# Kernel optimization log

Measured on AMD Instinct MI355X. Metric: run time of the kernel, lower is better.

Reference implementation:

```python
import jax, jax.numpy as jnp
import numpy as np

N_NODES = 20000
N_EDGES = 320000
N_GRAPHS = 512
IN_FEATS = 128
HID = 256
RDKIT_IN = 2048
RDK_H1, RDK_H2 = 1024, 512
COMB_H1, COMB_H2 = 1024, 512
N_TASKS = 1
EPS = 1e-5


def _lin(k, fan_in, fan_out):
    return jax.random.normal(k, (fan_in, fan_out), jnp.float32) / np.float32(np.sqrt(fan_in))


def setup_inputs() -> dict:
    key = jax.random.key(0)
    ks = jax.random.split(key, 24)
    inp = {}
    inp["node_feats"] = jax.random.normal(ks[0], (N_NODES, IN_FEATS), jnp.float32)
    inp["rdkit_feats"] = jax.random.normal(ks[1], (N_GRAPHS, RDKIT_IN), jnp.float32)
    inp["src"] = jax.random.randint(ks[2], (N_EDGES,), 0, N_NODES, dtype=jnp.int32)
    inp["dst"] = jax.random.randint(ks[3], (N_EDGES,), 0, N_NODES, dtype=jnp.int32)
    # sorted graph ids; first N_GRAPHS entries guarantee every graph has >=1 node
    gid = jnp.concatenate([jnp.arange(N_GRAPHS, dtype=jnp.int32),
                           jax.random.randint(ks[4], (N_NODES - N_GRAPHS,), 0, N_GRAPHS, dtype=jnp.int32)])
    inp["node_gid"] = jnp.sort(gid)
    # GCN layer params (GraphConv W,b + residual Linear + BatchNorm gamma/beta)
    dims = [(IN_FEATS, HID), (HID, HID)]
    for i, (fi, fo) in enumerate(dims, start=1):
        inp[f"W{i}"] = _lin(ks[4 + 4 * i], fi, fo)
        inp[f"b{i}"] = jnp.zeros((fo,), jnp.float32)
        inp[f"rW{i}"] = _lin(ks[5 + 4 * i], fi, fo)
        inp[f"rb{i}"] = jnp.zeros((fo,), jnp.float32)
        inp[f"g{i}"] = jnp.ones((fo,), jnp.float32)
        inp[f"be{i}"] = jnp.zeros((fo,), jnp.float32)
    inp["aw_W"] = _lin(ks[16], HID, 1)
    inp["aw_b"] = jnp.zeros((1,), jnp.float32)
    inp["rk_W1"] = _lin(ks[17], RDKIT_IN, RDK_H1)
    inp["rk_b1"] = jnp.zeros((RDK_H1,), jnp.float32)
    inp["rk_W2"] = _lin(ks[18], RDK_H1, RDK_H2)
    inp["rk_b2"] = jnp.zeros((RDK_H2,), jnp.float32)
    comb_in = RDK_H2 + 2 * HID
    inp["c_W1"] = _lin(ks[19], comb_in, COMB_H1)
    inp["c_b1"] = jnp.zeros((COMB_H1,), jnp.float32)
    inp["c_W2"] = _lin(ks[20], COMB_H1, COMB_H2)
    inp["c_b2"] = jnp.zeros((COMB_H2,), jnp.float32)
    inp["c_W3"] = _lin(ks[21], COMB_H2, N_TASKS)
    inp["c_b3"] = jnp.zeros((N_TASKS,), jnp.float32)
    return inp


def _gcn_layer(h, src, dst, W, b, rW, rb, g, be):
    # GraphConv, norm='none': sum incoming messages of (X W), then bias + relu
    m = h @ W                                                    # [N, out]
    agg = jax.ops.segment_sum(m[src], dst, num_segments=h.shape[0])
    new = jax.nn.relu(agg + b)
    # residual Linear with activation (dgllife GCNLayer)
    new = new + jax.nn.relu(h @ rW + rb)
    # BatchNorm1d over nodes (training-mode batch stats; dropout in eval = identity)
    mu = new.mean(axis=0)
    var = new.var(axis=0)
    return g * (new - mu) * jax.lax.rsqrt(var + EPS) + be


def reference(node_feats, rdkit_feats, src, dst, node_gid,
              W1, b1, rW1, rb1, g1, be1,
              W2, b2, rW2, rb2, g2, be2,
              aw_W, aw_b, rk_W1, rk_b1, rk_W2, rk_b2,
              c_W1, c_b1, c_W2, c_b2, c_W3, c_b3):
    h = _gcn_layer(node_feats, src, dst, W1, b1, rW1, rb1, g1, be1)
    h = _gcn_layer(h, src, dst, W2, b2, rW2, rb2, g2, be2)
    # WeightedSumAndMax readout
    w = jax.nn.sigmoid(h @ aw_W + aw_b)                          # [N, 1]
    hg_sum = jax.ops.segment_sum(h * w, node_gid, num_segments=N_GRAPHS)
    hg_max = jax.ops.segment_max(h, node_gid, num_segments=N_GRAPHS)
    graph_feats = jnp.concatenate([hg_sum, hg_max], axis=1)       # [B, 2*HID]
    # RDKit encoder MLP
    r = jax.nn.relu(rdkit_feats @ rk_W1 + rk_b1)
    r = jax.nn.relu(r @ rk_W2 + rk_b2)
    z = jnp.concatenate([graph_feats, r], axis=1)
    z = jax.nn.relu(z @ c_W1 + c_b1)
    z = jax.nn.relu(z @ c_W2 + c_b2)
    return z @ c_W3 + c_b3                                       # [B, n_tasks]
```

## Files before the change

kernel.cpp:

```cpp
#include <hip/hip_runtime.h>
#include <hip/hip_bf16.h>
#include <cstdint>
#include <cstddef>

#define N_NODES 20000
#define N_EDGES 320000
#define N_GRAPHS 512
#define IN_FEATS 128
#define HID 256

typedef __bf16 bhalf;
typedef __bf16 bhalf8 __attribute__((ext_vector_type(8)));
typedef __bf16 bhalf4 __attribute__((ext_vector_type(4)));
typedef __bf16 bhalf2 __attribute__((ext_vector_type(2)));
typedef float f32x4 __attribute__((ext_vector_type(4)));

template<int RELU, int OUTBF16>
__global__ __launch_bounds__(256) void gemm_mfma(const bhalf* __restrict__ A,
                                                 const bhalf* __restrict__ Bt,
                                                 void* __restrict__ Cv,
                                                 const float* __restrict__ bias,
                                                 int M, int K, int ldc)
{
    __shared__ bhalf As[64 * 64];
    __shared__ bhalf Bs[64 * 64];

    const int t = threadIdx.x;
    const int lane = t & 63, wid = t >> 6;
    const int wm0 = (wid >> 1) * 32, wn0 = (wid & 1) * 32;
    const int m0 = blockIdx.y * 64, n0 = blockIdx.x * 64;
    const int S = gridDim.z, kz = blockIdx.z;
    const int Ks = K / S;

    const int srow = t >> 2;
    const int sc0 = (t & 3) << 3;

    f32x4 acc[2][2] = {};
    uint4 ra0, ra1, rb0, rb1;

    const bool mok = (m0 + srow) < M;
    const bhalf* Abase = A + (size_t)(m0 + srow) * K + (size_t)kz * Ks;
    const bhalf* Bbase = Bt + (size_t)(n0 + srow) * K + (size_t)kz * Ks;

    ra0 = mok ? *(const uint4*)(Abase + sc0)      : make_uint4(0u,0u,0u,0u);
    ra1 = mok ? *(const uint4*)(Abase + sc0 + 32) : make_uint4(0u,0u,0u,0u);
    rb0 = *(const uint4*)(Bbase + sc0);
    rb1 = *(const uint4*)(Bbase + sc0 + 32);

    const int swz = (srow & 7) << 3;
    for (int k0 = 0; k0 < Ks; k0 += 64) {
        __syncthreads();
        *(uint4*)&As[srow * 64 + (sc0 ^ swz)]        = ra0;
        *(uint4*)&As[srow * 64 + ((sc0 + 32) ^ swz)] = ra1;
        *(uint4*)&Bs[srow * 64 + (sc0 ^ swz)]        = rb0;
        *(uint4*)&Bs[srow * 64 + ((sc0 + 32) ^ swz)] = rb1;
        __syncthreads();
        if (k0 + 64 < Ks) {
            const bhalf* An = Abase + k0 + 64;
            const bhalf* Bn = Bbase + k0 + 64;
            ra0 = mok ? *(const uint4*)(An + sc0)      : make_uint4(0u,0u,0u,0u);
            ra1 = mok ? *(const uint4*)(An + sc0 + 32) : make_uint4(0u,0u,0u,0u);
            rb0 = *(const uint4*)(Bn + sc0);
            rb1 = *(const uint4*)(Bn + sc0 + 32);
        }
#pragma unroll
        for (int kb = 0; kb < 2; ++kb) {
            const int kc = kb * 32 + (lane >> 4) * 8;
            bhalf8 af[2], bfr[2];
#pragma unroll
            for (int i = 0; i < 2; ++i) {
                int rA = wm0 + i * 16 + (lane & 15);
                af[i] = *(const bhalf8*)&As[rA * 64 + (kc ^ ((rA & 7) << 3))];
                int rB = wn0 + i * 16 + (lane & 15);
                bfr[i] = *(const bhalf8*)&Bs[rB * 64 + (kc ^ ((rB & 7) << 3))];
            }
#pragma unroll
            for (int mi = 0; mi < 2; ++mi)
#pragma unroll
                for (int ni = 0; ni < 2; ++ni)
                    acc[mi][ni] = __builtin_amdgcn_mfma_f32_16x16x32_bf16(
                        af[mi], bfr[ni], acc[mi][ni], 0, 0, 0);
        }
    }

#pragma unroll
    for (int mi = 0; mi < 2; ++mi)
#pragma unroll
        for (int ni = 0; ni < 2; ++ni) {
            int col = n0 + wn0 + ni * 16 + (lane & 15);
            f32x4 v = acc[mi][ni];
            if (S > 1) {
#pragma unroll
                for (int r = 0; r < 4; ++r) {
                    int row = m0 + wm0 + mi * 16 + (lane >> 4) * 4 + r;
                    if (row < M)
                        ((float*)Cv)[((size_t)kz * M + row) * ldc + col] = v[r];
                }
            } else {
                float bb = bias ? bias[col] : 0.f;
#pragma unroll
                for (int r = 0; r < 4; ++r) {
                    int row = m0 + wm0 + mi * 16 + (lane >> 4) * 4 + r;
                    if (row < M) {
                        float x = v[r] + bb;
                        if (RELU) x = fmaxf(x, 0.f);
                        if (OUTBF16) ((bhalf*)Cv)[(size_t)row * ldc + col] = (bhalf)x;
                        else         ((float*)Cv)[(size_t)row * ldc + col] = x;
                    }
                }
            }
        }
}

__global__ __launch_bounds__(256) void gcn_gemm_fused(const bhalf* __restrict__ Aagg,
                                                      const bhalf* __restrict__ Ax,
                                                      const bhalf* __restrict__ BW,
                                                      const bhalf* __restrict__ BrW,
                                                      const float* __restrict__ b,
                                                      const float* __restrict__ rb,
                                                      bhalf* __restrict__ vout,
                                                      float* __restrict__ stats,
                                                      int M, int K)
{
    __shared__ bhalf As[64 * 64];
    __shared__ bhalf Bs[64 * 64];
    __shared__ float ssum[64], ssq[64];

    const int t = threadIdx.x;
    const int lane = t & 63, wid = t >> 6;
    const int wm0 = (wid >> 1) * 32, wn0 = (wid & 1) * 32;
    const int m0 = blockIdx.y * 64, n0 = blockIdx.x * 64;

    const int srow = t >> 2;
    const int sc0 = (t & 3) << 3;
    const int nk = K >> 6;

    f32x4 accM[2][2] = {};
    f32x4 accR[2][2] = {};
    uint4 ra0, ra1, rb0, rb1;

    const bool mok = (m0 + srow) < M;
    const bhalf* A0r = Aagg + (size_t)(m0 + srow) * K;
    const bhalf* A1r = Ax + (size_t)(m0 + srow) * K;
    const bhalf* B0r = BW + (size_t)(n0 + srow) * K;
    const bhalf* B1r = BrW + (size_t)(n0 + srow) * K;

    ra0 = mok ? *(const uint4*)(A0r + sc0)      : make_uint4(0u,0u,0u,0u);
    ra1 = mok ? *(const uint4*)(A0r + sc0 + 32) : make_uint4(0u,0u,0u,0u);
    rb0 = *(const uint4*)(B0r + sc0);
    rb1 = *(const uint4*)(B0r + sc0 + 32);

    const int swz = (srow & 7) << 3;
    const int total = 2 * nk;
    for (int ii = 0; ii < total; ++ii) {
        __syncthreads();
        *(uint4*)&As[srow * 64 + (sc0 ^ swz)]        = ra0;
        *(uint4*)&As[srow * 64 + ((sc0 + 32) ^ swz)] = ra1;
        *(uint4*)&Bs[srow * 64 + (sc0 ^ swz)]        = rb0;
        *(uint4*)&Bs[srow * 64 + ((sc0 + 32) ^ swz)] = rb1;
        __syncthreads();
        int jj = ii + 1;
        if (jj < total) {
            bool seln = jj >= nk;
            int kk = (seln ? jj - nk : jj) << 6;
            const bhalf* Ab = (seln ? A1r : A0r) + kk;
            const bhalf* Bb = (seln ? B1r : B0r) + kk;
            ra0 = mok ? *(const uint4*)(Ab + sc0)      : make_uint4(0u,0u,0u,0u);
            ra1 = mok ? *(const uint4*)(Ab + sc0 + 32) : make_uint4(0u,0u,0u,0u);
            rb0 = *(const uint4*)(Bb + sc0);
            rb1 = *(const uint4*)(Bb + sc0 + 32);
        }
        const bool selc = ii >= nk;
#pragma unroll
        for (int kb = 0; kb < 2; ++kb) {
            const int kc = kb * 32 + (lane >> 4) * 8;
            bhalf8 af[2], bfr[2];
#pragma unroll
            for (int i = 0; i < 2; ++i) {
                int rA = wm0 + i * 16 + (lane & 15);
                af[i] = *(const bhalf8*)&As[rA * 64 + (kc ^ ((rA & 7) << 3))];
                int rB = wn0 + i * 16 + (lane & 15);
                bfr[i] = *(const bhalf8*)&Bs[rB * 64 + (kc ^ ((rB & 7) << 3))];
            }
            if (!selc) {
#pragma unroll
                for (int mi = 0; mi < 2; ++mi)
#pragma unroll
                    for (int ni = 0; ni < 2; ++ni)
                        accM[mi][ni] = __builtin_amdgcn_mfma_f32_16x16x32_bf16(
                            af[mi], bfr[ni], accM[mi][ni], 0, 0, 0);
            } else {
#pragma unroll
                for (int mi = 0; mi < 2; ++mi)
#pragma unroll
                    for (int ni = 0; ni < 2; ++ni)
                        accR[mi][ni] = __builtin_amdgcn_mfma_f32_16x16x32_bf16(
                            af[mi], bfr[ni], accR[mi][ni], 0, 0, 0);
            }
        }
    }

    if (t < 64) { ssum[t] = 0.f; ssq[t] = 0.f; }
    __syncthreads();
    float sloc[2] = {0.f, 0.f}, s2loc[2] = {0.f, 0.f};
#pragma unroll
    for (int ni = 0; ni < 2; ++ni) {
        int cl = wn0 + ni * 16 + (lane & 15);
        int c = n0 + cl;
        float bb = b[c], rbb = rb[c];
#pragma unroll
        for (int mi = 0; mi < 2; ++mi) {
            f32x4 a0v = accM[mi][ni], a1v = accR[mi][ni];
#pragma unroll
            for (int r = 0; r < 4; ++r) {
                int row = m0 + wm0 + mi * 16 + (lane >> 4) * 4 + r;
                if (row < M) {
                    float x = fmaxf(a0v[r] + bb, 0.f) + fmaxf(a1v[r] + rbb, 0.f);
                    vout[(size_t)row * HID + c] = (bhalf)x;
                    sloc[ni] += x;
                    s2loc[ni] += x * x;
                }
            }
        }
        atomicAdd(&ssum[cl], sloc[ni]);
        atomicAdd(&ssq[cl], s2loc[ni]);
    }
    __syncthreads();
    if (t < 64) {
        atomicAdd(&stats[n0 + t], ssum[t]);
        atomicAdd(&stats[HID + n0 + t], ssq[t]);
    }
}

template<int RELU, int OUTBF16>
__global__ __launch_bounds__(256) void splitk_combine(const float* __restrict__ part,
                                                      int S, int M, int N, int ldo,
                                                      const float* __restrict__ bias,
                                                      void* __restrict__ outv)
{
    int i = blockIdx.x * blockDim.x + threadIdx.x;
    int n4 = N >> 2;
    if (i >= M * n4) return;
    int row = i / n4, c4 = (i - row * n4) << 2;
    float4 s = make_float4(0.f, 0.f, 0.f, 0.f);
    for (int z = 0; z < S; ++z) {
        float4 p = *(const float4*)(part + ((size_t)z * M + row) * N + c4);
        s.x += p.x; s.y += p.y; s.z += p.z; s.w += p.w;
    }
    float4 bb = *(const float4*)(bias + c4);
    s.x += bb.x; s.y += bb.y; s.z += bb.z; s.w += bb.w;
    if (RELU) {
        s.x = fmaxf(s.x, 0.f); s.y = fmaxf(s.y, 0.f);
        s.z = fmaxf(s.z, 0.f); s.w = fmaxf(s.w, 0.f);
    }
    if (OUTBF16) {
        bhalf4 o = {(bhalf)s.x, (bhalf)s.y, (bhalf)s.z, (bhalf)s.w};
        *(bhalf4*)((bhalf*)outv + (size_t)row * ldo + c4) = o;
    } else {
        *(float4*)((float*)outv + (size_t)row * ldo + c4) = s;
    }
}

__global__ __launch_bounds__(128) void splitk_combine_dot(const float* __restrict__ part,
                                                          int S, int M, int N,
                                                          const float* __restrict__ bias,
                                                          const float* __restrict__ W3,
                                                          const float* __restrict__ b3,
                                                          float* __restrict__ out)
{
    int row = blockIdx.x, t = threadIdx.x;
    int c4 = t << 2;
    float4 s = make_float4(0.f, 0.f, 0.f, 0.f);
    for (int z = 0; z < S; ++z) {
        float4 p = *(const float4*)(part + ((size_t)z * M + row) * N + c4);
        s.x += p.x; s.y += p.y; s.z += p.z; s.w += p.w;
    }
    float4 bb = *(const float4*)(bias + c4);
    float4 w = *(const float4*)(W3 + c4);
    float d = fmaxf(s.x + bb.x, 0.f) * w.x + fmaxf(s.y + bb.y, 0.f) * w.y
            + fmaxf(s.z + bb.z, 0.f) * w.z + fmaxf(s.w + bb.w, 0.f) * w.w;
#pragma unroll
    for (int off = 32; off > 0; off >>= 1) d += __shfl_xor(d, off);
    __shared__ float ws2[2];
    if ((t & 63) == 0) ws2[t >> 6] = d;
    __syncthreads();
    if (t == 0) out[row] = ws2[0] + ws2[1] + b3[0];
}

struct WEnt { const float* src; bhalf* dst; int K; int N; int tiles_end; };
struct WTab { WEnt e[8]; };

__global__ __launch_bounds__(256) void wconv_batch(WTab tab)
{
    __shared__ float tile[32][33];
    int tb = blockIdx.x;
    int idx = 0;
#pragma unroll
    for (int i = 0; i < 8; ++i)
        if (tb >= tab.e[i].tiles_end) idx = i + 1;
    const WEnt& E = tab.e[idx];
    int t0 = idx ? tab.e[idx - 1].tiles_end : 0;
    int lt = tb - t0;
    int tX = E.N >> 5;
    int bx = (lt % tX) << 5;
    int by = (lt / tX) << 5;
    int tx = threadIdx.x & 31, ty = threadIdx.x >> 5;
#pragma unroll
    for (int i = 0; i < 32; i += 8)
        tile[ty + i][tx] = E.src[(size_t)(by + ty + i) * E.N + bx + tx];
    __syncthreads();
#pragma unroll
    for (int i = 0; i < 32; i += 8)
        E.dst[(size_t)(bx + ty + i) * E.K + by + tx] = (bhalf)tile[tx][ty + i];
}

__global__ void conv_batch(const float* __restrict__ a, bhalf* __restrict__ oa, int n4a,
                           const float* __restrict__ b, bhalf* __restrict__ ob, int n4b)
{
    int i = blockIdx.x * blockDim.x + threadIdx.x;
    const float* s; bhalf* d; int j;
    if (i < n4a) { s = a; d = oa; j = i; }
    else { j = i - n4a; if (j >= n4b) return; s = b; d = ob; }
    float4 v = ((const float4*)s)[j];
    bhalf4 o = {(bhalf)v.x, (bhalf)v.y, (bhalf)v.z, (bhalf)v.w};
    ((bhalf4*)d)[j] = o;
}

__global__ void csr_count(const int* __restrict__ dst, int* __restrict__ counts)
{
    int e = blockIdx.x * blockDim.x + threadIdx.x;
    if (e >= N_EDGES) return;
    atomicAdd(&counts[dst[e]], 1);
}

__global__ __launch_bounds__(256) void csr_scan_a(const int* __restrict__ counts,
                                                  int* __restrict__ bsum)
{
    int i = blockIdx.x * 256 + threadIdx.x;
    int v = (i < N_NODES) ? counts[i] : 0;
#pragma unroll
    for (int off = 32; off > 0; off >>= 1) v += __shfl_down(v, off);
    __shared__ int ws[4];
    if ((threadIdx.x & 63) == 0) ws[threadIdx.x >> 6] = v;
    __syncthreads();
    if (threadIdx.x == 0) bsum[blockIdx.x] = ws[0] + ws[1] + ws[2] + ws[3];
}

__global__ __launch_bounds__(128) void csr_scan_b(int* __restrict__ bsum, int nb)
{
    __shared__ int tmp[128];
    int t = threadIdx.x;
    tmp[t] = (t < nb) ? bsum[t] : 0;
    __syncthreads();
    if (t == 0) {
        int run = 0;
        for (int i = 0; i < nb; ++i) { int c = tmp[i]; tmp[i] = run; run += c; }
    }
    __syncthreads();
    if (t < nb) bsum[t] = tmp[t];
}

__global__ __launch_bounds__(256) void csr_scan_c(const int* __restrict__ counts,
                                                  const int* __restrict__ bsum,
                                                  int* __restrict__ offsets)
{
    int t = threadIdx.x, b = blockIdx.x;
    int i = b * 256 + t;
    int v = (i < N_NODES) ? counts[i] : 0;
    int x = v;
#pragma unroll
    for (int off = 1; off < 64; off <<= 1) {
        int y = __shfl_up(x, off);
        if ((t & 63) >= off) x += y;
    }
    __shared__ int wsum[4];
    if ((t & 63) == 63) wsum[t >> 6] = x;
    __syncthreads();
    int add = bsum[b];
    for (int w = 0; w < (t >> 6); ++w) add += wsum[w];
    int excl = x - v + add;
    if (i < N_NODES) offsets[i] = excl;
    if (i == N_NODES - 1) offsets[N_NODES] = excl + v;
}

__global__ void csr_fill(const int* __restrict__ src, const int* __restrict__ dst,
                         const int* __restrict__ offsets, int* __restrict__ cursor,
                         int* __restrict__ eidx)
{
    int e = blockIdx.x * blockDim.x + threadIdx.x;
    if (e >= N_EDGES) return;
    int d = dst[e];
    int slot = offsets[d] + atomicAdd(&cursor[d], 1);
    eidx[slot] = src[e];
}

__global__ void csr_sort_wave(const int* __restrict__ offsets, int* __restrict__ eidx)
{
    int gidx = blockIdx.x * blockDim.x + threadIdx.x;
    int n = gidx >> 6, lane = gidx & 63;
    if (n >= N_NODES) return;
    int lo = offsets[n], hi = offsets[n + 1];
    int cnt = hi - lo;
    if (cnt <= 1) return;
    if (cnt <= 64) {
        int v = (lane < cnt) ? eidx[lo + lane] : 0x7fffffff;
        int rank = 0;
        for (int j = 0; j < cnt; ++j) {
            int vj = __shfl(v, j);
            if (vj < v || (vj == v && j < lane)) ++rank;
        }
        if (lane < cnt) eidx[lo + rank] = v;
    } else if (lane == 0) {
        for (int i = lo + 1; i < hi; ++i) {
            int v = eidx[i]; int j = i - 1;
            while (j >= lo && eidx[j] > v) { eidx[j + 1] = eidx[j]; --j; }
            eidx[j + 1] = v;
        }
    }
}

template<int COLS>
__global__ __launch_bounds__(256) void edge_gather_b(const bhalf* __restrict__ m,
                                                     const int* __restrict__ offsets,
                                                     const int* __restrict__ eidx,
                                                     bhalf* __restrict__ agg)
{
    int gidx = blockIdx.x * blockDim.x + threadIdx.x;
    int n = gidx >> 6, lane = gidx & 63;
    if (n >= N_NODES) return;
    int lo = offsets[n], hi = offsets[n + 1];
    if (COLS == 256) {
        const bhalf* base = m + lane * 4;
        float4 acc = make_float4(0.f, 0.f, 0.f, 0.f);
        int i = lo;
        for (; i + 2 <= hi; i += 2) {
            bhalf4 v0 = *(const bhalf4*)(base + (size_t)eidx[i] * COLS);
            bhalf4 v1 = *(const bhalf4*)(base + (size_t)eidx[i + 1] * COLS);
            acc.x += (float)v0.x + (float)v1.x;
            acc.y += (float)v0.y + (float)v1.y;
            acc.z += (float)v0.z + (float)v1.z;
            acc.w += (float)v0.w + (float)v1.w;
        }
        if (i < hi) {
            bhalf4 v0 = *(const bhalf4*)(base + (size_t)eidx[i] * COLS);
            acc.x += (float)v0.x; acc.y += (float)v0.y;
            acc.z += (float)v0.z; acc.w += (float)v0.w;
        }
        bhalf4 o = {(bhalf)acc.x, (bhalf)acc.y, (bhalf)acc.z, (bhalf)acc.w};
        *(bhalf4*)(agg + (size_t)n * COLS + lane * 4) = o;
    } else {
        const bhalf* base = m + lane * 2;
        float ax = 0.f, ay = 0.f;
        int i = lo;
        for (; i + 2 <= hi; i += 2) {
            bhalf2 v0 = *(const bhalf2*)(base + (size_t)eidx[i] * COLS);
            bhalf2 v1 = *(const bhalf2*)(base + (size_t)eidx[i + 1] * COLS);
            ax += (float)v0.x + (float)v1.x;
            ay += (float)v0.y + (float)v1.y;
        }
        if (i < hi) {
            bhalf2 v0 = *(const bhalf2*)(base + (size_t)eidx[i] * COLS);
            ax += (float)v0.x; ay += (float)v0.y;
        }
        bhalf2 o = {(bhalf)ax, (bhalf)ay};
        *(bhalf2*)(agg + (size_t)n * COLS + lane * 2) = o;
    }
}

template<int MODE>
__global__ __launch_bounds__(256) void bn_row(const bhalf* __restrict__ v,
                                              const float* __restrict__ stats,
                                              float inv_n,
                                              const float* __restrict__ g,
                                              const float* __restrict__ be,
                                              bhalf* __restrict__ outb,
                                              const float* __restrict__ awW,
                                              const float* __restrict__ awb,
                                              float* __restrict__ w)
{
    int gidx = blockIdx.x * blockDim.x + threadIdx.x;
    int n = gidx >> 6, lane = gidx & 63;
    if (n >= N_NODES) return;
    int col = lane * 4;
    bhalf4 vv = *(const bhalf4*)(v + (size_t)n * HID + col);
    float4 sm = *(const float4*)(stats + col);
    float4 sq = *(const float4*)(stats + HID + col);
    float4 gg = *(const float4*)(g + col);
    float4 bb = *(const float4*)(be + col);
    float mux = sm.x * inv_n, muy = sm.y * inv_n, muz = sm.z * inv_n, muw = sm.w * inv_n;
    float rsx = rsqrtf(sq.x * inv_n - mux * mux + 1e-5f);
    float rsy = rsqrtf(sq.y * inv_n - muy * muy + 1e-5f);
    float rsz = rsqrtf(sq.z * inv_n - muz * muz + 1e-5f);
    float rsw = rsqrtf(sq.w * inv_n - muw * muw + 1e-5f);
    float4 o;
    o.x = gg.x * ((float)vv.x - mux) * rsx + bb.x;
    o.y = gg.y * ((float)vv.y - muy) * rsy + bb.y;
    o.z = gg.z * ((float)vv.z - muz) * rsz + bb.z;
    o.w = gg.w * ((float)vv.w - muw) * rsw + bb.w;
    bhalf4 ob = {(bhalf)o.x, (bhalf)o.y, (bhalf)o.z, (bhalf)o.w};
    *(bhalf4*)(outb + (size_t)n * HID + col) = ob;
    if (MODE == 1) {
        float4 wv = *(const float4*)(awW + col);
        float d = o.x * wv.x + o.y * wv.y + o.z * wv.z + o.w * wv.w;
#pragma unroll
        for (int off = 32; off > 0; off >>= 1) d += __shfl_xor(d, off);
        if (lane == 0) w[n] = 1.f / (1.f + expf(-(d + awb[0])));
    }
}

__global__ __launch_bounds__(256) void readout(const bhalf* __restrict__ h,
                                               const float* __restrict__ w,
                                               const int* __restrict__ gid,
                                               bhalf* __restrict__ z)
{
    int g = blockIdx.x, col = threadIdx.x;
    int lo = 0, hi = N_NODES;
    while (lo < hi) { int mid = (lo + hi) >> 1; if (gid[mid] < g) lo = mid + 1; else hi = mid; }
    int start = lo;
    hi = N_NODES;
    while (lo < hi) { int mid = (lo + hi) >> 1; if (gid[mid] <= g) lo = mid + 1; else hi = mid; }
    int end = lo;
    float s = 0.f, mx = -INFINITY;
    for (int n = start; n < end; ++n) {
        float v = (float)h[(size_t)n * HID + col];
        s = fmaf(v, w[n], s);
        mx = fmaxf(mx, v);
    }
    z[(size_t)g * 1024 + col] = (bhalf)s;
    z[(size_t)g * 1024 + HID + col] = (bhalf)mx;
}

extern "C" void kernel_launch(void* const* d_in, const int* in_sizes, int n_in,
                              void* d_out, int out_size, void* d_ws, size_t ws_size,
                              hipStream_t stream)
{
    (void)in_sizes; (void)n_in; (void)out_size; (void)ws_size;

    const float* node_feats = (const float*)d_in[0];
    const float* rdkit      = (const float*)d_in[1];
    const int*   src        = (const int*)d_in[2];
    const int*   dst        = (const int*)d_in[3];
    const int*   gid        = (const int*)d_in[4];
    const float* W1  = (const float*)d_in[5];
    const float* b1  = (const float*)d_in[6];
    const float* rW1 = (const float*)d_in[7];
    const float* rb1 = (const float*)d_in[8];
    const float* g1  = (const float*)d_in[9];
    const float* be1 = (const float*)d_in[10];
    const float* W2  = (const float*)d_in[11];
    const float* b2  = (const float*)d_in[12];
    const float* rW2 = (const float*)d_in[13];
    const float* rb2 = (const float*)d_in[14];
    const float* g2  = (const float*)d_in[15];
    const float* be2 = (const float*)d_in[16];
    const float* aw_W  = (const float*)d_in[17];
    const float* aw_b  = (const float*)d_in[18];
    const float* rk_W1 = (const float*)d_in[19];
    const float* rk_b1 = (const float*)d_in[20];
    const float* rk_W2 = (const float*)d_in[21];
    const float* rk_b2 = (const float*)d_in[22];
    const float* c_W1  = (const float*)d_in[23];
    const float* c_b1  = (const float*)d_in[24];
    const float* c_W2  = (const float*)d_in[25];
    const float* c_b2  = (const float*)d_in[26];
    const float* c_W3  = (const float*)d_in[27];
    const float* c_b3  = (const float*)d_in[28];

    float* out = (float*)d_out;

    const size_t NODE = (size_t)N_NODES * HID;
    bhalf* nfb   = (bhalf*)d_ws;
    bhalf* h1b   = nfb + (size_t)N_NODES * IN_FEATS;
    bhalf* h2b   = h1b + NODE;
    bhalf* aggb  = h2b + NODE;
    bhalf* vb    = aggb + NODE;
    bhalf* W1cat = vb + NODE;
    bhalf* W2cat = W1cat + 512 * 128;
    bhalf* rkW1t = W2cat + 512 * 256;
    bhalf* rkW2t = rkW1t + 2048 * 1024;
    bhalf* cW1t  = rkW2t + 1024 * 512;
    bhalf* cW2t  = cW1t + 1024 * 1024;
    bhalf* rdkb  = cW2t + 1024 * 512;
    float* stats1 = (float*)(rdkb + 512 * 2048);
    float* stats2 = stats1 + 512;
    float* wbuf   = stats2 + 512;
    int*   counts  = (int*)(wbuf + N_NODES);
    int*   cursor  = counts + N_NODES;
    int*   offsets = cursor + N_NODES;
    int*   eidx    = offsets + N_NODES + 1;
    int*   bsum    = eidx + N_EDGES;
    bhalf* rkhb  = (bhalf*)(bsum + 128);
    bhalf* zb    = rkhb + 512 * 1024;
    bhalf* ch1b  = zb + 512 * 1024;
    float* spart = (float*)(ch1b + 512 * 1024);

    dim3 blk(256);
    const int EPB = (N_EDGES + 255) / 256;
    const int NPB = (N_NODES + 255) / 256;
    const int NWAVE = (N_NODES * 64) / 256;
    dim3 gfused(HID / 64, (N_NODES + 63) / 64);

    WTab tab;
    tab.e[0] = {W1,    W1cat,             128, 256,   32};
    tab.e[1] = {rW1,   W1cat + 256 * 128, 128, 256,   64};
    tab.e[2] = {W2,    W2cat,             256, 256,  128};
    tab.e[3] = {rW2,   W2cat + 256 * 256, 256, 256,  192};
    tab.e[4] = {rk_W1, rkW1t,            2048, 1024, 2240};
    tab.e[5] = {rk_W2, rkW2t,            1024, 512,  2752};
    tab.e[6] = {c_W1,  cW1t,             1024, 1024, 3776};
    tab.e[7] = {c_W2,  cW2t,             1024, 512,  4288};
    wconv_batch<<<4288, blk, 0, stream>>>(tab);
    {
        int n4a = N_NODES * IN_FEATS / 4, n4b = 512 * 2048 / 4;
        conv_batch<<<(n4a + n4b + 255) / 256, blk, 0, stream>>>(node_feats, nfb, n4a,
                                                                rdkit, rdkb, n4b);
    }

    hipMemsetAsync(counts, 0, 2 * N_NODES * sizeof(int), stream);
    hipMemsetAsync(stats1, 0, 1024 * sizeof(float), stream);

    csr_count<<<EPB, blk, 0, stream>>>(dst, counts);
    csr_scan_a<<<NPB, blk, 0, stream>>>(counts, bsum);
    csr_scan_b<<<1, 128, 0, stream>>>(bsum, NPB);
    csr_scan_c<<<NPB, blk, 0, stream>>>(counts, bsum, offsets);
    csr_fill<<<EPB, blk, 0, stream>>>(src, dst, offsets, cursor, eidx);
    csr_sort_wave<<<NWAVE, blk, 0, stream>>>(offsets, eidx);

    edge_gather_b<IN_FEATS><<<NWAVE, blk, 0, stream>>>(nfb, offsets, eidx, aggb);
    gcn_gemm_fused<<<gfused, blk, 0, stream>>>(aggb, nfb, W1cat, W1cat + 256 * 128,
                                               b1, rb1, vb, stats1, N_NODES, IN_FEATS);
    bn_row<0><<<NWAVE, blk, 0, stream>>>(vb, stats1, 1.0f / N_NODES, g1, be1,
                                         h1b, nullptr, nullptr, nullptr);

    edge_gather_b<HID><<<NWAVE, blk, 0, stream>>>(h1b, offsets, eidx, aggb);
    gcn_gemm_fused<<<gfused, blk, 0, stream>>>(aggb, h1b, W2cat, W2cat + 256 * 256,
                                               b2, rb2, vb, stats2, N_NODES, HID);
    bn_row<1><<<NWAVE, blk, 0, stream>>>(vb, stats2, 1.0f / N_NODES, g2, be2,
                                         h2b, aw_W, aw_b, wbuf);

    readout<<<N_GRAPHS, HID, 0, stream>>>(h2b, wbuf, gid, zb);

    gemm_mfma<0,0><<<dim3(16, 8, 8), blk, 0, stream>>>(rdkb, rkW1t, spart, nullptr,
                                                       512, 2048, 1024);
    splitk_combine<1,1><<<512, blk, 0, stream>>>(spart, 8, 512, 1024, 1024, rk_b1, rkhb);
    gemm_mfma<0,0><<<dim3(8, 8, 8), blk, 0, stream>>>(rkhb, rkW2t, spart, nullptr,
                                                      512, 1024, 512);
    splitk_combine<1,1><<<256, blk, 0, stream>>>(spart, 8, 512, 512, 1024, rk_b2, zb + 512);

    gemm_mfma<0,0><<<dim3(16, 8, 4), blk, 0, stream>>>(zb, cW1t, spart, nullptr,
                                                       512, 1024, 1024);
    splitk_combine<1,1><<<512, blk, 0, stream>>>(spart, 4, 512, 1024, 1024, c_b1, ch1b);
    gemm_mfma<0,0><<<dim3(8, 8, 8), blk, 0, stream>>>(ch1b, cW2t, spart, nullptr,
                                                      512, 1024, 512);
    splitk_combine_dot<<<512, 128, 0, stream>>>(spart, 8, 512, 512, c_b2, c_W3, c_b3, out);
}
```

Before: 258.8 us.

## Merge prep kernels and memsets, fold scan stage, split layer-2 gather across two waves

Weight transposes, input conversions and the zeroing of counters and stats now run in one prep kernel instead of two kernels plus two memsets; the buffer layout is reordered so the zeroed regions are contiguous. The single-block scan stage is folded into the final scan kernel, where each block sums the block totals it needs. The layer-2 edge gather now uses two waves per node, each covering half the columns, to expose more memory parallelism. Both gathers are unrolled by four. This cuts launch count and serial gaps, at the cost of redundant prefix sums per block and more waves in the layer-2 gather.

```diff
diff --git a/kernel.cpp b/kernel.cpp
--- a/kernel.cpp
+++ b/kernel.cpp
@@ -288,42 +288,52 @@
 }
 
 struct WEnt { const float* src; bhalf* dst; int K; int N; int tiles_end; };
-struct WTab { WEnt e[8]; };
-
-__global__ __launch_bounds__(256) void wconv_batch(WTab tab)
+struct PrepTab {
+    WEnt e[8];
+    const float* ca; bhalf* coa; int n4a;
+    const float* cb; bhalf* cob; int n4b;
+    uint4* zbase; int zn;
+};
+
+#define WTILES 4288
+#define CONVB  3524
+
+__global__ __launch_bounds__(256) void prep_batch(PrepTab tab)
 {
     __shared__ float tile[32][33];
     int tb = blockIdx.x;
-    int idx = 0;
-#pragma unroll
-    for (int i = 0; i < 8; ++i)
-        if (tb >= tab.e[i].tiles_end) idx = i + 1;
-    const WEnt& E = tab.e[idx];
-    int t0 = idx ? tab.e[idx - 1].tiles_end : 0;
-    int lt = tb - t0;
-    int tX = E.N >> 5;
-    int bx = (lt % tX) << 5;
-    int by = (lt / tX) << 5;
-    int tx = threadIdx.x & 31, ty = threadIdx.x >> 5;
-#pragma unroll
-    for (int i = 0; i < 32; i += 8)
-        tile[ty + i][tx] = E.src[(size_t)(by + ty + i) * E.N + bx + tx];
-    __syncthreads();
-#pragma unroll
-    for (int i = 0; i < 32; i += 8)
-        E.dst[(size_t)(bx + ty + i) * E.K + by + tx] = (bhalf)tile[tx][ty + i];
-}
-
-__global__ void conv_batch(const float* __restrict__ a, bhalf* __restrict__ oa, int n4a,
-                           const float* __restrict__ b, bhalf* __restrict__ ob, int n4b)
-{
-    int i = blockIdx.x * blockDim.x + threadIdx.x;
-    const float* s; bhalf* d; int j;
-    if (i < n4a) { s = a; d = oa; j = i; }
-    else { j = i - n4a; if (j >= n4b) return; s = b; d = ob; }
-    float4 v = ((const float4*)s)[j];
-    bhalf4 o = {(bhalf)v.x, (bhalf)v.y, (bhalf)v.z, (bhalf)v.w};
-    ((bhalf4*)d)[j] = o;
+    int t = threadIdx.x;
+    if (tb < WTILES) {
+        int idx = 0;
+#pragma unroll
+        for (int i = 0; i < 8; ++i)
+            if (tb >= tab.e[i].tiles_end) idx = i + 1;
+        const WEnt& E = tab.e[idx];
+        int t0 = idx ? tab.e[idx - 1].tiles_end : 0;
+        int lt = tb - t0;
+        int tX = E.N >> 5;
+        int bx = (lt % tX) << 5;
+        int by = (lt / tX) << 5;
+        int tx = t & 31, ty = t >> 5;
+#pragma unroll
+        for (int i = 0; i < 32; i += 8)
+            tile[ty + i][tx] = E.src[(size_t)(by + ty + i) * E.N + bx + tx];
+        __syncthreads();
+#pragma unroll
+        for (int i = 0; i < 32; i += 8)
+            E.dst[(size_t)(bx + ty + i) * E.K + by + tx] = (bhalf)tile[tx][ty + i];
+    } else if (tb < WTILES + CONVB) {
+        int i = (tb - WTILES) * 256 + t;
+        const float* s; bhalf* d; int j;
+        if (i < tab.n4a) { s = tab.ca; d = tab.coa; j = i; }
+        else { j = i - tab.n4a; if (j >= tab.n4b) return; s = tab.cb; d = tab.cob; }
+        float4 v = ((const float4*)s)[j];
+        bhalf4 o = {(bhalf)v.x, (bhalf)v.y, (bhalf)v.z, (bhalf)v.w};
+        ((bhalf4*)d)[j] = o;
+    } else {
+        int j = (tb - WTILES - CONVB) * 256 + t;
+        if (j < tab.zn) tab.zbase[j] = make_uint4(0u, 0u, 0u, 0u);
+    }
 }
 
 __global__ void csr_count(const int* __restrict__ dst, int* __restrict__ counts)
@@ -346,22 +356,8 @@
     if (threadIdx.x == 0) bsum[blockIdx.x] = ws[0] + ws[1] + ws[2] + ws[3];
 }
 
-__global__ __launch_bounds__(128) void csr_scan_b(int* __restrict__ bsum, int nb)
-{
-    __shared__ int tmp[128];
-    int t = threadIdx.x;
-    tmp[t] = (t < nb) ? bsum[t] : 0;
-    __syncthreads();
-    if (t == 0) {
-        int run = 0;
-        for (int i = 0; i < nb; ++i) { int c = tmp[i]; tmp[i] = run; run += c; }
-    }
-    __syncthreads();
-    if (t < nb) bsum[t] = tmp[t];
-}
-
 __global__ __launch_bounds__(256) void csr_scan_c(const int* __restrict__ counts,
-                                                  const int* __restrict__ bsum,
+                                                  const int* __restrict__ bsum, int nb,
                                                   int* __restrict__ offsets)
 {
     int t = threadIdx.x, b = blockIdx.x;
@@ -374,9 +370,18 @@
         if ((t & 63) >= off) x += y;
     }
     __shared__ int wsum[4];
+    __shared__ int tmp[128];
+    __shared__ int addsh;
     if ((t & 63) == 63) wsum[t >> 6] = x;
+    if (t < 128) tmp[t] = (t < nb) ? bsum[t] : 0;
     __syncthreads();
-    int add = bsum[b];
+    if (t == 0) {
+        int a = 0;
+        for (int j = 0; j < b; ++j) a += tmp[j];
+        addsh = a;
+    }
+    __syncthreads();
+    int add = addsh;
     for (int w = 0; w < (t >> 6); ++w) add += wsum[w];
     int excl = x - v + add;
     if (i < N_NODES) offsets[i] = excl;
@@ -419,52 +424,62 @@
     }
 }
 
-template<int COLS>
-__global__ __launch_bounds__(256) void edge_gather_b(const bhalf* __restrict__ m,
-                                                     const int* __restrict__ offsets,
-                                                     const int* __restrict__ eidx,
-                                                     bhalf* __restrict__ agg)
+__global__ __launch_bounds__(256) void edge_gather1(const bhalf* __restrict__ m,
+                                                    const int* __restrict__ offsets,
+                                                    const int* __restrict__ eidx,
+                                                    bhalf* __restrict__ agg)
 {
     int gidx = blockIdx.x * blockDim.x + threadIdx.x;
     int n = gidx >> 6, lane = gidx & 63;
     if (n >= N_NODES) return;
     int lo = offsets[n], hi = offsets[n + 1];
-    if (COLS == 256) {
-        const bhalf* base = m + lane * 4;
-        float4 acc = make_float4(0.f, 0.f, 0.f, 0.f);
-        int i = lo;
-        for (; i + 2 <= hi; i += 2) {
-            bhalf4 v0 = *(const bhalf4*)(base + (size_t)eidx[i] * COLS);
-            bhalf4 v1 = *(const bhalf4*)(base + (size_t)eidx[i + 1] * COLS);
-            acc.x += (float)v0.x + (float)v1.x;
-            acc.y += (float)v0.y + (float)v1.y;
-            acc.z += (float)v0.z + (float)v1.z;
-            acc.w += (float)v0.w + (float)v1.w;
-        }
-        if (i < hi) {
-            bhalf4 v0 = *(const bhalf4*)(base + (size_t)eidx[i] * COLS);
-            acc.x += (float)v0.x; acc.y += (float)v0.y;
-            acc.z += (float)v0.z; acc.w += (float)v0.w;
-        }
-        bhalf4 o = {(bhalf)acc.x, (bhalf)acc.y, (bhalf)acc.z, (bhalf)acc.w};
-        *(bhalf4*)(agg + (size_t)n * COLS + lane * 4) = o;
-    } else {
-        const bhalf* base = m + lane * 2;
-        float ax = 0.f, ay = 0.f;
-        int i = lo;
-        for (; i + 2 <= hi; i += 2) {
-            bhalf2 v0 = *(const bhalf2*)(base + (size_t)eidx[i] * COLS);
-            bhalf2 v1 = *(const bhalf2*)(base + (size_t)eidx[i + 1] * COLS);
-            ax += (float)v0.x + (float)v1.x;
-            ay += (float)v0.y + (float)v1.y;
-        }
-        if (i < hi) {
-            bhalf2 v0 = *(const bhalf2*)(base + (size_t)eidx[i] * COLS);
-            ax += (float)v0.x; ay += (float)v0.y;
-        }
-        bhalf2 o = {(bhalf)ax, (bhalf)ay};
-        *(bhalf2*)(agg + (size_t)n * COLS + lane * 2) = o;
-    }
+    const bhalf* base = m + lane * 2;
+    float ax = 0.f, ay = 0.f;
+    int i = lo;
+    for (; i + 4 <= hi; i += 4) {
+        bhalf2 v0 = *(const bhalf2*)(base + (size_t)eidx[i] * IN_FEATS);
+        bhalf2 v1 = *(const bhalf2*)(base + (size_t)eidx[i + 1] * IN_FEATS);
+        bhalf2 v2 = *(const bhalf2*)(base + (size_t)eidx[i + 2] * IN_FEATS);
+        bhalf2 v3 = *(const bhalf2*)(base + (size_t)eidx[i + 3] * IN_FEATS);
+        ax += ((float)v0.x + (float)v1.x) + ((float)v2.x + (float)v3.x);
+        ay += ((float)v0.y + (float)v1.y) + ((float)v2.y + (float)v3.y);
+    }
+    for (; i < hi; ++i) {
+        bhalf2 v0 = *(const bhalf2*)(base + (size_t)eidx[i] * IN_FEATS);
+        ax += (float)v0.x; ay += (float)v0.y;
+    }
+    bhalf2 o = {(bhalf)ax, (bhalf)ay};
+    *(bhalf2*)(agg + (size_t)n * IN_FEATS + lane * 2) = o;
+}
+
+__global__ __launch_bounds__(256) void edge_gather2(const bhalf* __restrict__ m,
+                                                    const int* __restrict__ offsets,
+                                                    const int* __restrict__ eidx,
+                                                    bhalf* __restrict__ agg)
+{
+    int gidx = blockIdx.x * blockDim.x + threadIdx.x;
+    int w = gidx >> 6, lane = gidx & 63;
+    int n = w >> 1, half = w & 1;
+    if (n >= N_NODES) return;
+    int lo = offsets[n], hi = offsets[n + 1];
+    int coff = half * 128 + lane * 2;
+    const bhalf* base = m + coff;
+    float ax = 0.f, ay = 0.f;
+    int i = lo;
+    for (; i + 4 <= hi; i += 4) {
+        bhalf2 v0 = *(const bhalf2*)(base + (size_t)eidx[i] * HID);
+        bhalf2 v1 = *(const bhalf2*)(base + (size_t)eidx[i + 1] * HID);
+        bhalf2 v2 = *(const bhalf2*)(base + (size_t)eidx[i + 2] * HID);
+        bhalf2 v3 = *(const bhalf2*)(base + (size_t)eidx[i + 3] * HID);
+        ax += ((float)v0.x + (float)v1.x) + ((float)v2.x + (float)v3.x);
+        ay += ((float)v0.y + (float)v1.y) + ((float)v2.y + (float)v3.y);
+    }
+    for (; i < hi; ++i) {
+        bhalf2 v0 = *(const bhalf2*)(base + (size_t)eidx[i] * HID);
+        ax += (float)v0.x; ay += (float)v0.y;
+    }
+    bhalf2 o = {(bhalf)ax, (bhalf)ay};
+    *(bhalf2*)(agg + (size_t)n * HID + coff) = o;
 }
 
 template<int MODE>
@@ -583,10 +598,10 @@
     bhalf* rdkb  = cW2t + 1024 * 512;
     float* stats1 = (float*)(rdkb + 512 * 2048);
     float* stats2 = stats1 + 512;
-    float* wbuf   = stats2 + 512;
-    int*   counts  = (int*)(wbuf + N_NODES);
-    int*   cursor  = counts + N_NODES;
-    int*   offsets = cursor + N_NODES;
+    int*   counts = (int*)(stats2 + 512);
+    int*   cursor = counts + N_NODES;
+    float* wbuf   = (float*)(cursor + N_NODES);
+    int*   offsets = (int*)(wbuf + N_NODES);
     int*   eidx    = offsets + N_NODES + 1;
     int*   bsum    = eidx + N_EDGES;
     bhalf* rkhb  = (bhalf*)(bsum + 128);
@@ -598,9 +613,10 @@
     const int EPB = (N_EDGES + 255) / 256;
     const int NPB = (N_NODES + 255) / 256;
     const int NWAVE = (N_NODES * 64) / 256;
+    const int NWAVE2 = (N_NODES * 128) / 256;
     dim3 gfused(HID / 64, (N_NODES + 63) / 64);
 
-    WTab tab;
+    PrepTab tab;
     tab.e[0] = {W1,    W1cat,             128, 256,   32};
     tab.e[1] = {rW1,   W1cat + 256 * 128, 128, 256,   64};
     tab.e[2] = {W2,    W2cat,             256, 256,  128};
@@ -609,30 +625,26 @@
     tab.e[5] = {rk_W2, rkW2t,            1024, 512,  2752};
     tab.e[6] = {c_W1,  cW1t,             1024, 1024, 3776};
     tab.e[7] = {c_W2,  cW2t,             1024, 512,  4288};
-    wconv_batch<<<4288, blk, 0, stream>>>(tab);
-    {
-        int n4a = N_NODES * IN_FEATS / 4, n4b = 512 * 2048 / 4;
-        conv_batch<<<(n4a + n4b + 255) / 256, blk, 0, stream>>>(node_feats, nfb, n4a,
-                                                                rdkit, rdkb, n4b);
-    }
-
-    hipMemsetAsync(counts, 0, 2 * N_NODES * sizeof(int), stream);
-    hipMemsetAsync(stats1, 0, 1024 * sizeof(float), stream);
+    tab.ca = node_feats; tab.coa = nfb;  tab.n4a = N_NODES * IN_FEATS / 4;
+    tab.cb = rdkit;      tab.cob = rdkb; tab.n4b = 512 * 2048 / 4;
+    tab.zbase = (uint4*)stats1;
+    tab.zn = (1024 + 2 * N_NODES) / 4;
+    const int ZB = (tab.zn + 255) / 256;
+    prep_batch<<<WTILES + CONVB + ZB, blk, 0, stream>>>(tab);
 
     csr_count<<<EPB, blk, 0, stream>>>(dst, counts);
     csr_scan_a<<<NPB, blk, 0, stream>>>(counts, bsum);
-    csr_scan_b<<<1, 128, 0, stream>>>(bsum, NPB);
-    csr_scan_c<<<NPB, blk, 0, stream>>>(counts, bsum, offsets);
+    csr_scan_c<<<NPB, blk, 0, stream>>>(counts, bsum, NPB, offsets);
     csr_fill<<<EPB, blk, 0, stream>>>(src, dst, offsets, cursor, eidx);
     csr_sort_wave<<<NWAVE, blk, 0, stream>>>(offsets, eidx);
 
-    edge_gather_b<IN_FEATS><<<NWAVE, blk, 0, stream>>>(nfb, offsets, eidx, aggb);
+    edge_gather1<<<NWAVE, blk, 0, stream>>>(nfb, offsets, eidx, aggb);
     gcn_gemm_fused<<<gfused, blk, 0, stream>>>(aggb, nfb, W1cat, W1cat + 256 * 128,
                                                b1, rb1, vb, stats1, N_NODES, IN_FEATS);
     bn_row<0><<<NWAVE, blk, 0, stream>>>(vb, stats1, 1.0f / N_NODES, g1, be1,
                                          h1b, nullptr, nullptr, nullptr);
 
-    edge_gather_b<HID><<<NWAVE, blk, 0, stream>>>(h1b, offsets, eidx, aggb);
+    edge_gather2<<<NWAVE2, blk, 0, stream>>>(h1b, offsets, eidx, aggb);
     gcn_gemm_fused<<<gfused, blk, 0, stream>>>(aggb, h1b, W2cat, W2cat + 256 * 256,
                                                b2, rb2, vb, stats2, N_NODES, HID);
     bn_row<1><<<NWAVE, blk, 0, stream>>>(vb, stats2, 1.0f / N_NODES, g2, be2,
```

Result: faster. 249.5 us (-3.6%).
